# Kernel tuning notes

Hardware: AMD Instinct MI355X
Metric: run time of the kernel (lower is better)

Reference implementation:

```python
import jax, jax.numpy as jnp
import numpy as np

N_NODES = 8192
N_EDGES = 131072
EMB_NF = 256
IN_NODE_NF = 64
IN_EDGE_NF = 16


def setup_inputs() -> dict:
    key = jax.random.key(0)
    ks = jax.random.split(key, 8)
    node_emb = jax.random.normal(ks[0], (N_NODES, EMB_NF), dtype=jnp.float32)
    edge_emb = jax.random.normal(ks[1], (N_EDGES, EMB_NF), dtype=jnp.float32)
    # Linear head params (torch nn.Linear: y = x @ W.T + b)
    s = 1.0 / np.sqrt(EMB_NF)
    node_w = jax.random.uniform(ks[2], (IN_NODE_NF, EMB_NF), jnp.float32, -s, s)
    node_b = jax.random.uniform(ks[3], (IN_NODE_NF,), jnp.float32, -s, s)
    edge_w = jax.random.uniform(ks[4], (IN_EDGE_NF, EMB_NF), jnp.float32, -s, s)
    edge_b = jax.random.uniform(ks[5], (IN_EDGE_NF,), jnp.float32, -s, s)
    W = 0.5 * jnp.ones((1,), dtype=jnp.float32)
    b = 0.8 * jnp.ones((1,), dtype=jnp.float32)
    return {"node_emb": node_emb, "edge_emb": edge_emb,
            "node_w": node_w, "node_b": node_b,
            "edge_w": edge_w, "edge_b": edge_b,
            "W": W, "b": b}


def reference(node_emb, edge_emb, node_w, node_b, edge_w, edge_b, W, b):
    # Two linear decode heads
    recon_node_fs = node_emb @ node_w.T + node_b          # [N, in_node_nf]
    recon_edge_fs = edge_emb @ edge_w.T + edge_b          # [E, in_edge_nf]
    # Pairwise squared L2 distance: sum_d (x_i - x_j)^2 = |x_i|^2 + |x_j|^2 - 2 x_i.x_j
    sq = jnp.sum(node_emb * node_emb, axis=1)             # [N]
    d2 = sq[:, None] + sq[None, :] - 2.0 * (node_emb @ node_emb.T)  # [N, N]
    adj_pred = jax.nn.sigmoid(W[0] * d2 + b[0])           # [N, N]
    n = node_emb.shape[0]
    adj_pred = adj_pred * (1.0 - jnp.eye(n, dtype=adj_pred.dtype))  # remove self loops
    return (recon_node_fs, recon_edge_fs, adj_pred)
```

## Files before the change

### kernel.cpp

```cpp
#include <hip/hip_runtime.h>
#include <cstdint>
#include <cstddef>

#define NN 8192
#define NE 131072
#define EMB 256

typedef float f32x4 __attribute__((ext_vector_type(4)));
typedef __bf16 bf16x8 __attribute__((ext_vector_type(8)));

__device__ __forceinline__ unsigned short f2bf(float f) {
  unsigned u = __float_as_uint(f);
  u += 0x7fffu + ((u >> 16) & 1u);
  return (unsigned short)(u >> 16);
}

__device__ __forceinline__ void gload_lds16(const void* g, void* l) {
  __builtin_amdgcn_global_load_lds(
      (const __attribute__((address_space(1))) unsigned int*)g,
      (__attribute__((address_space(3))) unsigned int*)l, 16, 0, 0);
}

__global__ __launch_bounds__(256) void node_prep_kernel(const float* __restrict__ X,
                                                        const float* __restrict__ w,
                                                        const float* __restrict__ bias,
                                                        float* __restrict__ out,
                                                        unsigned short* __restrict__ Xb,
                                                        float* __restrict__ sq) {
  __shared__ float xs[16 * 260];
  int tid = threadIdx.x;
  int n0  = blockIdx.x * 16;
  int r   = tid >> 4, g = tid & 15;

  float s = 0.f;
  #pragma unroll
  for (int kc = 0; kc < 4; ++kc) {
    float4 v = *(const float4*)(X + (size_t)(n0 + r) * EMB + kc * 64 + g * 4);
    *(float4*)(&xs[r * 260 + kc * 64 + g * 4]) = v;
    s += v.x * v.x + v.y * v.y + v.z * v.z + v.w * v.w;
    ushort4 b;
    b.x = f2bf(v.x); b.y = f2bf(v.y); b.z = f2bf(v.z); b.w = f2bf(v.w);
    *(ushort4*)(Xb + (size_t)(n0 + r) * EMB + kc * 64 + g * 4) = b;
  }
  s += __shfl_xor(s, 1); s += __shfl_xor(s, 2);
  s += __shfl_xor(s, 4); s += __shfl_xor(s, 8);
  if (g == 0) sq[n0 + r] = s;
  __syncthreads();

  int o0 = g * 4;
  float acc[4] = {0.f, 0.f, 0.f, 0.f};
  #pragma unroll 4
  for (int k = 0; k < 256; k += 4) {
    float4 x = *(const float4*)(&xs[r * 260 + k]);
    #pragma unroll
    for (int oo = 0; oo < 4; ++oo) {
      float4 wv = *(const float4*)(w + (size_t)(o0 + oo) * EMB + k);
      acc[oo] = fmaf(x.x, wv.x, fmaf(x.y, wv.y, fmaf(x.z, wv.z, fmaf(x.w, wv.w, acc[oo]))));
    }
  }
  float4 o;
  o.x = acc[0] + bias[o0 + 0];
  o.y = acc[1] + bias[o0 + 1];
  o.z = acc[2] + bias[o0 + 2];
  o.w = acc[3] + bias[o0 + 3];
  *(float4*)(out + (size_t)(n0 + r) * 64 + o0) = o;
}

__global__ __launch_bounds__(256) void mega_kernel(const unsigned short* __restrict__ Xb,
                                                   const float* __restrict__ sq,
                                                   const float* __restrict__ Wp,
                                                   const float* __restrict__ bp,
                                                   float* __restrict__ adj_out,
                                                   const float* __restrict__ Xe,
                                                   const float* __restrict__ ew,
                                                   const float* __restrict__ eb,
                                                   float* __restrict__ edge_out) {
  __shared__ __align__(16) char smem[32768];
  int tid = threadIdx.x;
  int b   = blockIdx.x;
  int g   = b / 9, rem = b - g * 9;

  if (rem == 8) {
    float* lds = (float*)smem;
    int e0 = g * 256;
    int lr = tid >> 2, lc = (tid & 3) * 4;

    float4 v[4];
    #pragma unroll
    for (int q = 0; q < 4; ++q)
      v[q] = *(const float4*)(Xe + (size_t)(e0 + lr + q * 64) * EMB + lc);

    float acc[16];
    #pragma unroll
    for (int o = 0; o < 16; ++o) acc[o] = 0.f;

    for (int kc = 0; kc < 16; ++kc) {
      __syncthreads();
      #pragma unroll
      for (int q = 0; q < 4; ++q) {
        float* d = &lds[(lr + q * 64) * 17 + lc];
        d[0] = v[q].x; d[1] = v[q].y; d[2] = v[q].z; d[3] = v[q].w;
      }
      __syncthreads();
      if (kc < 15) {
        #pragma unroll
        for (int q = 0; q < 4; ++q)
          v[q] = *(const float4*)(Xe + (size_t)(e0 + lr + q * 64) * EMB + (kc + 1) * 16 + lc);
      }
      const float* wk0 = ew + kc * 16;
      #pragma unroll
      for (int k = 0; k < 16; ++k) {
        float x = lds[tid * 17 + k];
        #pragma unroll
        for (int o = 0; o < 16; ++o)
          acc[o] = fmaf(x, wk0[(size_t)o * EMB + k], acc[o]);
      }
    }
    #pragma unroll
    for (int o = 0; o < 16; ++o) acc[o] += eb[o];
    float4* dst = (float4*)(edge_out + (size_t)(e0 + tid) * 16);
    dst[0] = make_float4(acc[0], acc[1], acc[2], acc[3]);
    dst[1] = make_float4(acc[4], acc[5], acc[6], acc[7]);
    dst[2] = make_float4(acc[8], acc[9], acc[10], acc[11]);
    dst[3] = make_float4(acc[12], acc[13], acc[14], acc[15]);
    return;
  }

  int adjid = g * 8 + rem;
  int low3  = adjid & 7, q = adjid >> 3;
  int ti = low3 * 8 + (q & 7);
  int tj = ((q >> 6) & 7) * 8 + ((q >> 3) & 7);

  int wave = tid >> 6, lane = tid & 63;
  int wr = (wave >> 1) * 64;
  int wc = (wave & 1) * 64;
  int l15 = lane & 15, lg = lane >> 4;

  f32x4 acc[4][4] = {};

  int srow0 = wave * 32 + (lane >> 2);
  int sp    = lane & 3;

  const size_t rowA = (size_t)(ti * 128) * EMB;
  const size_t rowB = (size_t)(tj * 128) * EMB;

#define STAGE(BUF, KT)                                                          \
  {                                                                             \
    char* base = smem + (BUF) * 16384;                                          \
    int r0 = srow0, r1 = srow0 + 16;                                            \
    int c0 = (KT) * 32 + ((sp ^ ((r0 >> 1) & 3)) << 3);                         \
    int c1 = (KT) * 32 + ((sp ^ ((r1 >> 1) & 3)) << 3);                         \
    gload_lds16(Xb + rowA + (size_t)r0 * EMB + c0, base + wave * 2048);         \
    gload_lds16(Xb + rowA + (size_t)r1 * EMB + c1, base + wave * 2048 + 1024);  \
    gload_lds16(Xb + rowB + (size_t)r0 * EMB + c0, base + 8192 + wave * 2048);  \
    gload_lds16(Xb + rowB + (size_t)r1 * EMB + c1, base + 8192 + wave * 2048 + 1024); \
  }

  STAGE(0, 0)

  #pragma unroll
  for (int kt = 0; kt < 8; ++kt) {
    if (kt < 7) {
      STAGE((kt + 1) & 1, kt + 1)
      asm volatile("s_waitcnt vmcnt(4)" ::: "memory");
    } else {
      asm volatile("s_waitcnt vmcnt(0)" ::: "memory");
    }
    __builtin_amdgcn_sched_barrier(0);
    __builtin_amdgcn_s_barrier();
    __builtin_amdgcn_sched_barrier(0);

    const char* Ab = smem + (kt & 1) * 16384;
    const char* Bb = Ab + 8192;
    bf16x8 af[4], bfr[4];
    #pragma unroll
    for (int m = 0; m < 4; ++m) {
      int rr = wr + m * 16 + l15;
      af[m] = *(const bf16x8*)(Ab + rr * 64 + ((lg ^ ((rr >> 1) & 3)) << 4));
    }
    #pragma unroll
    for (int n = 0; n < 4; ++n) {
      int rr = wc + n * 16 + l15;
      bfr[n] = *(const bf16x8*)(Bb + rr * 64 + ((lg ^ ((rr >> 1) & 3)) << 4));
    }
    #pragma unroll
    for (int m = 0; m < 4; ++m)
      #pragma unroll
      for (int n = 0; n < 4; ++n)
        acc[m][n] = __builtin_amdgcn_mfma_f32_16x16x32_bf16(af[m], bfr[n], acc[m][n], 0, 0, 0);

    __builtin_amdgcn_sched_barrier(0);
    __builtin_amdgcn_s_barrier();
    __builtin_amdgcn_sched_barrier(0);
  }
#undef STAGE

  float W0 = Wp[0], b0 = bp[0];
  float w2 = -2.0f * W0;
  int col0 = tj * 128 + wc + l15;
  int row0 = ti * 128 + wr + (lg << 2);
  bool diag = (ti == tj);

  float aiW[16];
  #pragma unroll
  for (int m = 0; m < 4; ++m)
    #pragma unroll
    for (int rg = 0; rg < 4; ++rg)
      aiW[m * 4 + rg] = W0 * sq[row0 + m * 16 + rg];

  #pragma unroll
  for (int n = 0; n < 4; ++n) {
    int j = col0 + n * 16;
    float sjW = fmaf(W0, sq[j], b0);
    #pragma unroll
    for (int m = 0; m < 4; ++m) {
      #pragma unroll
      for (int rg = 0; rg < 4; ++rg) {
        float t = fmaf(w2, acc[m][n][rg], aiW[m * 4 + rg] + sjW);
        acc[m][n][rg] = __builtin_amdgcn_rcpf(1.0f + __expf(-t));
      }
      if (diag) {
        #pragma unroll
        for (int rg = 0; rg < 4; ++rg)
          if (row0 + m * 16 + rg == j) acc[m][n][rg] = 0.0f;
      }
      __builtin_nontemporal_store(acc[m][n],
          (f32x4*)(&adj_out[(size_t)j * NN + row0 + m * 16]));
    }
  }
}

extern "C" void kernel_launch(void* const* d_in, const int* in_sizes, int n_in,
                              void* d_out, int out_size, void* d_ws, size_t ws_size,
                              hipStream_t stream) {
  const float* node_emb = (const float*)d_in[0];
  const float* edge_emb = (const float*)d_in[1];
  const float* node_w   = (const float*)d_in[2];
  const float* node_b   = (const float*)d_in[3];
  const float* edge_w   = (const float*)d_in[4];
  const float* edge_b   = (const float*)d_in[5];
  const float* Wp       = (const float*)d_in[6];
  const float* bp       = (const float*)d_in[7];

  float* out      = (float*)d_out;
  float* node_out = out;
  float* edge_out = out + (size_t)NN * 64;
  float* adj_out  = out + (size_t)NN * 64 + (size_t)NE * 16;

  unsigned short* Xb = (unsigned short*)d_ws;
  float* sq = (float*)((char*)d_ws + (size_t)NN * EMB * 2);

  node_prep_kernel<<<dim3(512), dim3(256), 0, stream>>>(node_emb, node_w, node_b,
                                                        node_out, Xb, sq);
  mega_kernel<<<dim3(4608), dim3(256), 0, stream>>>(Xb, sq, Wp, bp, adj_out,
                                                    edge_emb, edge_w, edge_b, edge_out);
}
```

Before: 168.0 us.

## Split edge head out of fused kernel and retile adjacency GEMM to 256x64

Moves the edge linear head from the fused mega kernel into its own launch. The adjacency kernel now uses 256x64 tiles, with each wave computing 128x32, in place of 128x128. The block-to-tile mapping changes so that each group of blocks shares a strip of rows, and output stores become regular stores instead of nontemporal ones. The goal is better store locality into the transposed output, since each column j writes 256 contiguous floats, and simpler scheduling. The costs are an extra kernel launch, lower arithmetic intensity per tile, and losing the overlap between the edge work and the adjacency work.

Measured after the change: 246.2 us. 1.46x slower.

```diff
diff --git a/kernel.cpp b/kernel.cpp
--- a/kernel.cpp
+++ b/kernel.cpp
@@ -66,94 +66,92 @@
   *(float4*)(out + (size_t)(n0 + r) * 64 + o0) = o;
 }
 
-__global__ __launch_bounds__(256) void mega_kernel(const unsigned short* __restrict__ Xb,
-                                                   const float* __restrict__ sq,
-                                                   const float* __restrict__ Wp,
-                                                   const float* __restrict__ bp,
-                                                   float* __restrict__ adj_out,
-                                                   const float* __restrict__ Xe,
-                                                   const float* __restrict__ ew,
-                                                   const float* __restrict__ eb,
-                                                   float* __restrict__ edge_out) {
-  __shared__ __align__(16) char smem[32768];
+__global__ __launch_bounds__(256) void edge_head_kernel(const float* __restrict__ X,
+                                                        const float* __restrict__ w,
+                                                        const float* __restrict__ bias,
+                                                        float* __restrict__ out) {
+  __shared__ float xs[256 * 17];
   int tid = threadIdx.x;
-  int b   = blockIdx.x;
-  int g   = b / 9, rem = b - g * 9;
-
-  if (rem == 8) {
-    float* lds = (float*)smem;
-    int e0 = g * 256;
-    int lr = tid >> 2, lc = (tid & 3) * 4;
-
-    float4 v[4];
-    #pragma unroll
-    for (int q = 0; q < 4; ++q)
-      v[q] = *(const float4*)(Xe + (size_t)(e0 + lr + q * 64) * EMB + lc);
-
-    float acc[16];
-    #pragma unroll
-    for (int o = 0; o < 16; ++o) acc[o] = 0.f;
-
-    for (int kc = 0; kc < 16; ++kc) {
-      __syncthreads();
-      #pragma unroll
-      for (int q = 0; q < 4; ++q) {
-        float* d = &lds[(lr + q * 64) * 17 + lc];
-        d[0] = v[q].x; d[1] = v[q].y; d[2] = v[q].z; d[3] = v[q].w;
-      }
-      __syncthreads();
-      if (kc < 15) {
-        #pragma unroll
-        for (int q = 0; q < 4; ++q)
-          v[q] = *(const float4*)(Xe + (size_t)(e0 + lr + q * 64) * EMB + (kc + 1) * 16 + lc);
-      }
-      const float* wk0 = ew + kc * 16;
-      #pragma unroll
-      for (int k = 0; k < 16; ++k) {
-        float x = lds[tid * 17 + k];
-        #pragma unroll
-        for (int o = 0; o < 16; ++o)
-          acc[o] = fmaf(x, wk0[(size_t)o * EMB + k], acc[o]);
-      }
-    }
-    #pragma unroll
-    for (int o = 0; o < 16; ++o) acc[o] += eb[o];
-    float4* dst = (float4*)(edge_out + (size_t)(e0 + tid) * 16);
-    dst[0] = make_float4(acc[0], acc[1], acc[2], acc[3]);
-    dst[1] = make_float4(acc[4], acc[5], acc[6], acc[7]);
-    dst[2] = make_float4(acc[8], acc[9], acc[10], acc[11]);
-    dst[3] = make_float4(acc[12], acc[13], acc[14], acc[15]);
-    return;
-  }
-
-  int adjid = g * 8 + rem;
-  int low3  = adjid & 7, q = adjid >> 3;
-  int ti = low3 * 8 + (q & 7);
-  int tj = ((q >> 6) & 7) * 8 + ((q >> 3) & 7);
+  int e0  = blockIdx.x * 256;
+  int lr  = tid >> 2, lc = (tid & 3) * 4;
+
+  float4 v[4];
+  #pragma unroll
+  for (int q = 0; q < 4; ++q)
+    v[q] = *(const float4*)(X + (size_t)(e0 + lr + q * 64) * EMB + lc);
+
+  float acc[16];
+  #pragma unroll
+  for (int o = 0; o < 16; ++o) acc[o] = 0.f;
+
+  for (int kc = 0; kc < 16; ++kc) {
+    __syncthreads();
+    #pragma unroll
+    for (int q = 0; q < 4; ++q) {
+      float* d = &xs[(lr + q * 64) * 17 + lc];
+      d[0] = v[q].x; d[1] = v[q].y; d[2] = v[q].z; d[3] = v[q].w;
+    }
+    __syncthreads();
+    if (kc < 15) {
+      #pragma unroll
+      for (int q = 0; q < 4; ++q)
+        v[q] = *(const float4*)(X + (size_t)(e0 + lr + q * 64) * EMB + (kc + 1) * 16 + lc);
+    }
+    const float* wk0 = w + kc * 16;
+    #pragma unroll
+    for (int k = 0; k < 16; ++k) {
+      float x = xs[tid * 17 + k];
+      #pragma unroll
+      for (int o = 0; o < 16; ++o)
+        acc[o] = fmaf(x, wk0[(size_t)o * EMB + k], acc[o]);
+    }
+  }
+  #pragma unroll
+  for (int o = 0; o < 16; ++o) acc[o] += bias[o];
+  float4* dst = (float4*)(out + (size_t)(e0 + tid) * 16);
+  dst[0] = make_float4(acc[0], acc[1], acc[2], acc[3]);
+  dst[1] = make_float4(acc[4], acc[5], acc[6], acc[7]);
+  dst[2] = make_float4(acc[8], acc[9], acc[10], acc[11]);
+  dst[3] = make_float4(acc[12], acc[13], acc[14], acc[15]);
+}
+
+__global__ __launch_bounds__(256) void adj_kernel(const unsigned short* __restrict__ Xb,
+                                                  const float* __restrict__ sq,
+                                                  const float* __restrict__ Wp,
+                                                  const float* __restrict__ bp,
+                                                  float* __restrict__ adj_out) {
+  __shared__ __align__(16) char smem[40960];
+  int tid = threadIdx.x;
+  int b = blockIdx.x;
+  int x = b & 7, s = b >> 3;
+  int ti = x * 4 + (s >> 7);
+  int tj = s & 127;
 
   int wave = tid >> 6, lane = tid & 63;
-  int wr = (wave >> 1) * 64;
-  int wc = (wave & 1) * 64;
+  int wi = wave >> 1, wj = wave & 1;
   int l15 = lane & 15, lg = lane >> 4;
 
-  f32x4 acc[4][4] = {};
-
-  int srow0 = wave * 32 + (lane >> 2);
-  int sp    = lane & 3;
-
-  const size_t rowA = (size_t)(ti * 128) * EMB;
-  const size_t rowB = (size_t)(tj * 128) * EMB;
-
-#define STAGE(BUF, KT)                                                          \
-  {                                                                             \
-    char* base = smem + (BUF) * 16384;                                          \
-    int r0 = srow0, r1 = srow0 + 16;                                            \
-    int c0 = (KT) * 32 + ((sp ^ ((r0 >> 1) & 3)) << 3);                         \
-    int c1 = (KT) * 32 + ((sp ^ ((r1 >> 1) & 3)) << 3);                         \
-    gload_lds16(Xb + rowA + (size_t)r0 * EMB + c0, base + wave * 2048);         \
-    gload_lds16(Xb + rowA + (size_t)r1 * EMB + c1, base + wave * 2048 + 1024);  \
-    gload_lds16(Xb + rowB + (size_t)r0 * EMB + c0, base + 8192 + wave * 2048);  \
-    gload_lds16(Xb + rowB + (size_t)r1 * EMB + c1, base + 8192 + wave * 2048 + 1024); \
+  f32x4 acc[8][2] = {};
+
+  int srow = lane >> 2;
+  int sp   = lane & 3;
+
+  const size_t baseA = (size_t)(ti * 256) * EMB;
+  const size_t baseB = (size_t)(tj * 64) * EMB;
+
+#define STAGE(BUF, KT)                                                            \
+  {                                                                               \
+    char* Ab_ = smem + (BUF) * 20480;                                             \
+    char* Bb_ = Ab_ + 16384;                                                      \
+    _Pragma("unroll")                                                             \
+    for (int c = 0; c < 4; ++c) {                                                 \
+      int r = wave * 64 + c * 16 + srow;                                          \
+      int col = (KT) * 32 + ((sp ^ ((r >> 1) & 3)) << 3);                         \
+      gload_lds16(Xb + baseA + (size_t)r * EMB + col, Ab_ + wave * 4096 + c * 1024); \
+    }                                                                             \
+    int rb = wave * 16 + srow;                                                    \
+    int colb = (KT) * 32 + ((sp ^ ((rb >> 1) & 3)) << 3);                         \
+    gload_lds16(Xb + baseB + (size_t)rb * EMB + colb, Bb_ + wave * 1024);         \
   }
 
   STAGE(0, 0)
@@ -162,7 +160,7 @@
   for (int kt = 0; kt < 8; ++kt) {
     if (kt < 7) {
       STAGE((kt + 1) & 1, kt + 1)
-      asm volatile("s_waitcnt vmcnt(4)" ::: "memory");
+      asm volatile("s_waitcnt vmcnt(5)" ::: "memory");
     } else {
       asm volatile("s_waitcnt vmcnt(0)" ::: "memory");
     }
@@ -170,23 +168,23 @@
     __builtin_amdgcn_s_barrier();
     __builtin_amdgcn_sched_barrier(0);
 
-    const char* Ab = smem + (kt & 1) * 16384;
-    const char* Bb = Ab + 8192;
-    bf16x8 af[4], bfr[4];
-    #pragma unroll
-    for (int m = 0; m < 4; ++m) {
-      int rr = wr + m * 16 + l15;
+    const char* Ab = smem + (kt & 1) * 20480;
+    const char* Bb = Ab + 16384;
+    bf16x8 af[8], bfr[2];
+    #pragma unroll
+    for (int m = 0; m < 8; ++m) {
+      int rr = wi * 128 + m * 16 + l15;
       af[m] = *(const bf16x8*)(Ab + rr * 64 + ((lg ^ ((rr >> 1) & 3)) << 4));
     }
     #pragma unroll
-    for (int n = 0; n < 4; ++n) {
-      int rr = wc + n * 16 + l15;
-      bfr[n] = *(const bf16x8*)(Bb + rr * 64 + ((lg ^ ((rr >> 1) & 3)) << 4));
-    }
-    #pragma unroll
-    for (int m = 0; m < 4; ++m)
-      #pragma unroll
-      for (int n = 0; n < 4; ++n)
+    for (int n = 0; n < 2; ++n) {
+      int rj = wj * 32 + n * 16 + l15;
+      bfr[n] = *(const bf16x8*)(Bb + rj * 64 + ((lg ^ ((rj >> 1) & 3)) << 4));
+    }
+    #pragma unroll
+    for (int m = 0; m < 8; ++m)
+      #pragma unroll
+      for (int n = 0; n < 2; ++n)
         acc[m][n] = __builtin_amdgcn_mfma_f32_16x16x32_bf16(af[m], bfr[n], acc[m][n], 0, 0, 0);
 
     __builtin_amdgcn_sched_barrier(0);
@@ -197,35 +195,34 @@
 
   float W0 = Wp[0], b0 = bp[0];
   float w2 = -2.0f * W0;
-  int col0 = tj * 128 + wc + l15;
-  int row0 = ti * 128 + wr + (lg << 2);
-  bool diag = (ti == tj);
-
-  float aiW[16];
-  #pragma unroll
-  for (int m = 0; m < 4; ++m)
+  int i0base = ti * 256 + wi * 128 + (lg << 2);
+  int jbase  = tj * 64 + wj * 32 + l15;
+  bool dpos = ((tj >> 2) == ti);
+
+  float aiW[32];
+  #pragma unroll
+  for (int m = 0; m < 8; ++m)
     #pragma unroll
     for (int rg = 0; rg < 4; ++rg)
-      aiW[m * 4 + rg] = W0 * sq[row0 + m * 16 + rg];
-
-  #pragma unroll
-  for (int n = 0; n < 4; ++n) {
-    int j = col0 + n * 16;
+      aiW[m * 4 + rg] = W0 * sq[i0base + m * 16 + rg];
+
+  #pragma unroll
+  for (int n = 0; n < 2; ++n) {
+    int j = jbase + n * 16;
     float sjW = fmaf(W0, sq[j], b0);
     #pragma unroll
-    for (int m = 0; m < 4; ++m) {
+    for (int m = 0; m < 8; ++m) {
       #pragma unroll
       for (int rg = 0; rg < 4; ++rg) {
         float t = fmaf(w2, acc[m][n][rg], aiW[m * 4 + rg] + sjW);
         acc[m][n][rg] = __builtin_amdgcn_rcpf(1.0f + __expf(-t));
       }
-      if (diag) {
+      if (dpos) {
         #pragma unroll
         for (int rg = 0; rg < 4; ++rg)
-          if (row0 + m * 16 + rg == j) acc[m][n][rg] = 0.0f;
+          if (i0base + m * 16 + rg == j) acc[m][n][rg] = 0.0f;
       }
-      __builtin_nontemporal_store(acc[m][n],
-          (f32x4*)(&adj_out[(size_t)j * NN + row0 + m * 16]));
+      *(f32x4*)(&adj_out[(size_t)j * NN + i0base + m * 16]) = acc[m][n];
     }
   }
 }
@@ -252,6 +249,6 @@
 
   node_prep_kernel<<<dim3(512), dim3(256), 0, stream>>>(node_emb, node_w, node_b,
                                                         node_out, Xb, sq);
-  mega_kernel<<<dim3(4608), dim3(256), 0, stream>>>(Xb, sq, Wp, bp, adj_out,
-                                                    edge_emb, edge_w, edge_b, edge_out);
-}
+  edge_head_kernel<<<dim3(512), dim3(256), 0, stream>>>(edge_emb, edge_w, edge_b, edge_out);
+  adj_kernel<<<dim3(4096), dim3(256), 0, stream>>>(Xb, sq, Wp, bp, adj_out);
+}
```
